# Optimization experiments

Hardware: AMD Instinct MI355X
Metric: run time of the kernel (lower is better)

## Reference

```python
import jax, jax.numpy as jnp
import numpy as np

NUM_NODES = 10000
NODE_DIM = 128
EDGE_DIM = 128
HIDDEN_DIM = 128
OUT_DIM = 128
N_EDGES = 640000


def setup_inputs() -> dict:
    key = jax.random.key(0)
    k = jax.random.split(key, 8)
    x = jax.random.normal(k[0], (NUM_NODES, NODE_DIM), dtype=jnp.float32)
    edge_index = jax.random.randint(k[1], (2, N_EDGES), 0, NUM_NODES, dtype=jnp.int64)
    edge_attr = jax.random.normal(k[2], (N_EDGES, EDGE_DIM), dtype=jnp.float32)
    # node2edge linear: in = 2*node_dim + edge_dim
    s1 = 1.0 / np.sqrt(2 * NODE_DIM + EDGE_DIM)
    W1 = jax.random.uniform(k[3], (2 * NODE_DIM + EDGE_DIM, HIDDEN_DIM), jnp.float32, -s1, s1)
    b1 = jax.random.uniform(k[4], (HIDDEN_DIM,), jnp.float32, -s1, s1)
    # edge2node linear: in = hidden_dim + node_dim
    s2 = 1.0 / np.sqrt(HIDDEN_DIM + NODE_DIM)
    W2 = jax.random.uniform(k[5], (HIDDEN_DIM + NODE_DIM, OUT_DIM), jnp.float32, -s2, s2)
    b2 = jax.random.uniform(k[6], (OUT_DIM,), jnp.float32, -s2, s2)
    return {"x": x, "edge_index": edge_index, "edge_attr": edge_attr,
            "W1": W1, "b1": b1, "W2": W2, "b2": b2}


def reference(x, edge_index, edge_attr, W1, b1, W2, b2):
    src, dst = edge_index[0], edge_index[1]
    # Node2Edge: gather endpoints, concat with edge features, linear
    h_i = x[src]                                   # [E, node_dim]
    h_j = x[dst]                                   # [E, node_dim]
    inp_e = jnp.concatenate([h_i, h_j, edge_attr], axis=-1)  # [E, 2*nd+ed]
    h_edge = inp_e @ W1 + b1                       # [E, hidden]
    # Edge2Node: scatter-sum edge embeddings to target nodes (edge_index[1])
    agg = jax.ops.segment_sum(h_edge, dst, num_segments=NUM_NODES)  # [N, hidden]
    inp_n = jnp.concatenate([agg, x], axis=-1)     # [N, hidden+nd]
    h_node = inp_n @ W2 + b2                       # [N, out]
    return h_node
```

## Files before the change

kernel.cpp:

```cpp
#include <hip/hip_runtime.h>


#define NN 10000
#define ED 640000
#define D  128
#define NB 64
#define EPB (ED / NB)

typedef __bf16 bf16;
typedef bf16  bf16x8 __attribute__((ext_vector_type(8)));
typedef float f32x4  __attribute__((ext_vector_type(4)));

__device__ __forceinline__ bf16 f2b(float f) {
  unsigned u = __builtin_bit_cast(unsigned, f);
  u += 0x7fffu + ((u >> 16) & 1u);
  unsigned short h = (unsigned short)(u >> 16);
  return __builtin_bit_cast(bf16, h);
}

__device__ __forceinline__ bf16x8 bzero8() {
  bf16 z = __builtin_bit_cast(bf16, (unsigned short)0);
  bf16x8 v = {z, z, z, z, z, z, z, z};
  return v;
}

__global__ __launch_bounds__(256) void k_prep(const float* __restrict__ x,
                                              const float* __restrict__ W1,
                                              const float* __restrict__ W2,
                                              bf16* __restrict__ xb,
                                              bf16* __restrict__ W1p,
                                              bf16* __restrict__ W2p) {
  int id = blockIdx.x * 256 + threadIdx.x;
  if (id < 160000) {
    int i = id * 8;
    f32x4 a = *(const f32x4*)(x + i);
    f32x4 b = *(const f32x4*)(x + i + 4);
    bf16x8 h;
    h[0]=f2b(a[0]); h[1]=f2b(a[1]); h[2]=f2b(a[2]); h[3]=f2b(a[3]);
    h[4]=f2b(b[0]); h[5]=f2b(b[1]); h[6]=f2b(b[2]); h[7]=f2b(b[3]);
    *(bf16x8*)(xb + i) = h;
  } else if (id < 166144) {
    int o8 = id - 160000;
    int kb = o8 >> 9, rem = o8 & 511, t = rem >> 6, L = rem & 63;
    int col  = t * 16 + (L & 15);
    int row0 = kb * 32 + (L >> 4) * 8;
    bf16x8 h;
    #pragma unroll
    for (int j = 0; j < 8; j++) h[j] = f2b(W1[(row0 + j) * D + col]);
    *(bf16x8*)(W1p + o8 * 8) = h;
  } else if (id < 170240) {
    int o8 = id - 166144;
    int kb = o8 >> 9, rem = o8 & 511, t = rem >> 6, L = rem & 63;
    int col  = t * 16 + (L & 15);
    int row0 = kb * 32 + (L >> 4) * 8;
    bf16x8 h;
    #pragma unroll
    for (int j = 0; j < 8; j++) h[j] = f2b(W2[(row0 + j) * D + col]);
    *(bf16x8*)(W2p + o8 * 8) = h;
  }
}

__global__ __launch_bounds__(256) void k_hist(const int* __restrict__ dst,
                                              int* __restrict__ hist) {
  __shared__ __align__(16) int h[NN];
  int b = blockIdx.x, tid = threadIdx.x;
  int4 z4 = make_int4(0, 0, 0, 0);
  for (int i = tid; i < NN / 4; i += 256) ((int4*)h)[i] = z4;
  __syncthreads();
  const int4* d4 = (const int4*)(dst + b * EPB);
  for (int i = tid; i < EPB / 4; i += 256) {
    int4 dd = d4[i];
    atomicAdd(&h[dd.x], 1);
    atomicAdd(&h[dd.y], 1);
    atomicAdd(&h[dd.z], 1);
    atomicAdd(&h[dd.w], 1);
  }
  __syncthreads();
  int4* outp = (int4*)(hist + (size_t)b * NN);
  for (int i = tid; i < NN / 4; i += 256) outp[i] = ((const int4*)h)[i];
}

__global__ __launch_bounds__(256) void k_colscan(int* __restrict__ hist,
                                                 int* __restrict__ counts) {
  int v = blockIdx.x * 256 + threadIdx.x;
  if (v >= NN) return;
  int run = 0;
  #pragma unroll
  for (int b = 0; b < NB; b++) {
    int t = hist[b * NN + v];
    hist[b * NN + v] = run;
    run += t;
  }
  counts[v] = run;
}

__global__ __launch_bounds__(256) void k_scan(const int* __restrict__ counts,
                                              int* __restrict__ row_ptr) {
  __shared__ int part[256];
  int tid = threadIdx.x;
  const int CH = 40;
  int base = tid * CH;
  int loc[CH];
  if (base + CH <= NN) {
    #pragma unroll
    for (int i = 0; i < CH / 4; i++) {
      int4 t = *(const int4*)(counts + base + i * 4);
      loc[i*4] = t.x; loc[i*4+1] = t.y; loc[i*4+2] = t.z; loc[i*4+3] = t.w;
    }
  } else {
    #pragma unroll
    for (int i = 0; i < CH; i++) loc[i] = (base + i < NN) ? counts[base + i] : 0;
  }
  int sum = 0;
  #pragma unroll
  for (int i = 0; i < CH; i++) sum += loc[i];
  part[tid] = sum;
  __syncthreads();
  for (int off = 1; off < 256; off <<= 1) {
    int v = (tid >= off) ? part[tid - off] : 0;
    __syncthreads();
    part[tid] += v;
    __syncthreads();
  }
  int run = part[tid] - sum;
  if (base + CH <= NN) {
    #pragma unroll
    for (int i = 0; i < CH / 4; i++) {
      int4 t;
      t.x = run; run += loc[i*4];
      t.y = run; run += loc[i*4+1];
      t.z = run; run += loc[i*4+2];
      t.w = run; run += loc[i*4+3];
      *(int4*)(row_ptr + base + i * 4) = t;
    }
  } else {
    #pragma unroll
    for (int i = 0; i < CH; i++) {
      int idx = base + i;
      if (idx < NN) { row_ptr[idx] = run; run += loc[i]; }
    }
  }
  if (tid == 255) row_ptr[NN] = part[255];
}

__global__ __launch_bounds__(256) void k_fill(const int* __restrict__ src,
                                              const int* __restrict__ dst,
                                              const int* __restrict__ row_ptr,
                                              const int* __restrict__ hist,
                                              int2* __restrict__ csr) {
  __shared__ __align__(16) int rk[NN];
  int b = blockIdx.x, tid = threadIdx.x;
  int4 z4 = make_int4(0, 0, 0, 0);
  for (int i = tid; i < NN / 4; i += 256) ((int4*)rk)[i] = z4;
  __syncthreads();
  int base = b * EPB;
  const int* __restrict__ hb = hist + (size_t)b * NN;
  const int4* d4 = (const int4*)(dst + base);
  const int4* s4 = (const int4*)(src + base);
  for (int i = tid; i < EPB / 4; i += 256) {
    int4 dd = d4[i];
    int4 ss = s4[i];
    int e = base + i * 4;
    {
      int r = atomicAdd(&rk[dd.x], 1);
      csr[row_ptr[dd.x] + hb[dd.x] + r] = make_int2(e + 0, ss.x);
    }
    {
      int r = atomicAdd(&rk[dd.y], 1);
      csr[row_ptr[dd.y] + hb[dd.y] + r] = make_int2(e + 1, ss.y);
    }
    {
      int r = atomicAdd(&rk[dd.z], 1);
      csr[row_ptr[dd.z] + hb[dd.z] + r] = make_int2(e + 2, ss.z);
    }
    {
      int r = atomicAdd(&rk[dd.w], 1);
      csr[row_ptr[dd.w] + hb[dd.w] + r] = make_int2(e + 3, ss.w);
    }
  }
}

__global__ __launch_bounds__(256) void k_sum(const bf16*  __restrict__ xb,
                                             const float* __restrict__ ea,
                                             const int*   __restrict__ row_ptr,
                                             const int2*  __restrict__ csr,
                                             float* __restrict__ sx,
                                             float* __restrict__ sea) {
  int gwave = (blockIdx.x * 256 + threadIdx.x) >> 6;
  if (gwave >= NN) return;
  int lane = threadIdx.x & 63;
  int g = lane >> 4, l = lane & 15;
  int e0 = row_ptr[gwave], e1 = row_ptr[gwave + 1];

  f32x4 ax0 = {0.f,0.f,0.f,0.f}, ax1 = {0.f,0.f,0.f,0.f};
  f32x4 ae0 = {0.f,0.f,0.f,0.f}, ae1 = {0.f,0.f,0.f,0.f};

  #pragma unroll 2
  for (int e = e0 + g; e < e1; e += 4) {
    long long cp = __builtin_nontemporal_load((const long long*)(csr + e));
    int2 es = __builtin_bit_cast(int2, cp);
    const f32x4* ep = (const f32x4*)(ea + (size_t)es.x * D + l * 8);
    f32x4 f0 = __builtin_nontemporal_load(ep);
    f32x4 f1 = __builtin_nontemporal_load(ep + 1);
    bf16x8 hx = *(const bf16x8*)(xb + (size_t)es.y * D + l * 8);
    ax0[0] += (float)hx[0]; ax0[1] += (float)hx[1];
    ax0[2] += (float)hx[2]; ax0[3] += (float)hx[3];
    ax1[0] += (float)hx[4]; ax1[1] += (float)hx[5];
    ax1[2] += (float)hx[6]; ax1[3] += (float)hx[7];
    ae0 += f0;
    ae1 += f1;
  }
  #pragma unroll
  for (int i = 0; i < 4; i++) {
    ax0[i] += __shfl_xor(ax0[i], 16, 64); ax0[i] += __shfl_xor(ax0[i], 32, 64);
    ax1[i] += __shfl_xor(ax1[i], 16, 64); ax1[i] += __shfl_xor(ax1[i], 32, 64);
    ae0[i] += __shfl_xor(ae0[i], 16, 64); ae0[i] += __shfl_xor(ae0[i], 32, 64);
    ae1[i] += __shfl_xor(ae1[i], 16, 64); ae1[i] += __shfl_xor(ae1[i], 32, 64);
  }
  if (lane < 16) {
    float* px = sx  + (size_t)gwave * D + l * 8;
    float* pe = sea + (size_t)gwave * D + l * 8;
    *(f32x4*)px       = ax0;
    *(f32x4*)(px + 4) = ax1;
    *(f32x4*)pe       = ae0;
    *(f32x4*)(pe + 4) = ae1;
  }
}

__global__ __launch_bounds__(256) void k_out(const float* __restrict__ sx,
                                             const float* __restrict__ sea,
                                             const bf16*  __restrict__ xb,
                                             const bf16*  __restrict__ W1p,
                                             const bf16*  __restrict__ W2p,
                                             const float* __restrict__ b1,
                                             const float* __restrict__ b2,
                                             const int*   __restrict__ row_ptr,
                                             float* __restrict__ out) {
  __shared__ __align__(16) bf16 lds[64 * 392];
  int tid  = threadIdx.x;
  int wave = tid >> 6, lane = tid & 63, quad = lane >> 4, l16 = lane & 15;
  int n0 = blockIdx.x * 64;

  #pragma unroll
  for (int i = 0; i < 4; i++) {
    int m = (tid >> 4) + 16 * i;
    int v = n0 + m;
    int cl = tid & 15;
    float cntf = (v < NN) ? (float)(row_ptr[v + 1] - row_ptr[v]) : 0.f;
    #pragma unroll
    for (int j = 0; j < 3; j++) {
      int c = cl + 16 * j;
      bf16x8 h;
      if (v < NN) {
        if (j == 0) {
          const float* p = sx + (size_t)v * D + cl * 8;
          f32x4 f0 = *(const f32x4*)p, f1 = *(const f32x4*)(p + 4);
          h[0]=f2b(f0[0]); h[1]=f2b(f0[1]); h[2]=f2b(f0[2]); h[3]=f2b(f0[3]);
          h[4]=f2b(f1[0]); h[5]=f2b(f1[1]); h[6]=f2b(f1[2]); h[7]=f2b(f1[3]);
        } else if (j == 1) {
          bf16x8 hx = *(const bf16x8*)(xb + (size_t)v * D + cl * 8);
          #pragma unroll
          for (int k = 0; k < 8; k++) h[k] = f2b((float)hx[k] * cntf);
        } else {
          const float* p = sea + (size_t)v * D + cl * 8;
          f32x4 f0 = *(const f32x4*)p, f1 = *(const f32x4*)(p + 4);
          h[0]=f2b(f0[0]); h[1]=f2b(f0[1]); h[2]=f2b(f0[2]); h[3]=f2b(f0[3]);
          h[4]=f2b(f1[0]); h[5]=f2b(f1[1]); h[6]=f2b(f1[2]); h[7]=f2b(f1[3]);
        }
      } else h = bzero8();
      *(bf16x8*)&lds[m * 392 + c * 8] = h;
    }
  }
  __syncthreads();

  f32x4 acc[4][2];
  #pragma unroll
  for (int mt = 0; mt < 4; mt++)
    #pragma unroll
    for (int tt = 0; tt < 2; tt++) acc[mt][tt] = (f32x4){0.f, 0.f, 0.f, 0.f};

  #pragma unroll
  for (int kb = 0; kb < 12; kb++) {
    bf16x8 B0 = *(const bf16x8*)(W1p + ((kb * 8 + wave * 2 + 0) * 64 + lane) * 8);
    bf16x8 B1 = *(const bf16x8*)(W1p + ((kb * 8 + wave * 2 + 1) * 64 + lane) * 8);
    #pragma unroll
    for (int mt = 0; mt < 4; mt++) {
      bf16x8 a = *(const bf16x8*)&lds[(mt * 16 + l16) * 392 + kb * 32 + quad * 8];
      acc[mt][0] = __builtin_amdgcn_mfma_f32_16x16x32_bf16(a, B0, acc[mt][0], 0, 0, 0);
      acc[mt][1] = __builtin_amdgcn_mfma_f32_16x16x32_bf16(a, B1, acc[mt][1], 0, 0, 0);
    }
  }
  __syncthreads();

  #pragma unroll
  for (int tt = 0; tt < 2; tt++) {
    int col = wave * 32 + tt * 16 + l16;
    float bb = b1[col];
    #pragma unroll
    for (int mt = 0; mt < 4; mt++)
      #pragma unroll
      for (int r = 0; r < 4; r++) {
        int m = mt * 16 + quad * 4 + r;
        int v = n0 + m;
        float cntf = (v < NN) ? (float)(row_ptr[v + 1] - row_ptr[v]) : 0.f;
        lds[m * 264 + col] = f2b(acc[mt][tt][r] + cntf * bb);
      }
  }
  #pragma unroll
  for (int i = 0; i < 4; i++) {
    int m = (tid >> 4) + 16 * i;
    int c = tid & 15;
    int v = n0 + m;
    bf16x8 h = (v < NN) ? *(const bf16x8*)(xb + (size_t)v * D + c * 8) : bzero8();
    *(bf16x8*)&lds[m * 264 + 128 + c * 8] = h;
  }
  __syncthreads();

  f32x4 acc2[4][2];
  #pragma unroll
  for (int mt = 0; mt < 4; mt++)
    #pragma unroll
    for (int tt = 0; tt < 2; tt++) acc2[mt][tt] = (f32x4){0.f, 0.f, 0.f, 0.f};

  #pragma unroll
  for (int kb = 0; kb < 8; kb++) {
    bf16x8 B0 = *(const bf16x8*)(W2p + ((kb * 8 + wave * 2 + 0) * 64 + lane) * 8);
    bf16x8 B1 = *(const bf16x8*)(W2p + ((kb * 8 + wave * 2 + 1) * 64 + lane) * 8);
    #pragma unroll
    for (int mt = 0; mt < 4; mt++) {
      bf16x8 a = *(const bf16x8*)&lds[(mt * 16 + l16) * 264 + kb * 32 + quad * 8];
      acc2[mt][0] = __builtin_amdgcn_mfma_f32_16x16x32_bf16(a, B0, acc2[mt][0], 0, 0, 0);
      acc2[mt][1] = __builtin_amdgcn_mfma_f32_16x16x32_bf16(a, B1, acc2[mt][1], 0, 0, 0);
    }
  }

  #pragma unroll
  for (int tt = 0; tt < 2; tt++) {
    int col = wave * 32 + tt * 16 + l16;
    float bb = b2[col];
    #pragma unroll
    for (int mt = 0; mt < 4; mt++)
      #pragma unroll
      for (int r = 0; r < 4; r++) {
        int v = n0 + mt * 16 + quad * 4 + r;
        if (v < NN) out[(size_t)v * D + col] = acc2[mt][tt][r] + bb;
      }
  }
}

extern "C" void kernel_launch(void* const* d_in, const int* in_sizes, int n_in,
                              void* d_out, int out_size, void* d_ws, size_t ws_size,
                              hipStream_t stream) {
  const float* x  = (const float*)d_in[0];
  const int*   ei = (const int*)  d_in[1];
  const float* ea = (const float*)d_in[2];
  const float* W1 = (const float*)d_in[3];
  const float* b1 = (const float*)d_in[4];
  const float* W2 = (const float*)d_in[5];
  const float* b2 = (const float*)d_in[6];
  float* out = (float*)d_out;

  char* ws = (char*)d_ws;
  size_t off = 0;
  auto alloc = [&](size_t bytes) -> void* {
    void* p = ws + off;
    off += (bytes + 255) & ~(size_t)255;
    return p;
  };
  bf16*  xb      = (bf16*)alloc((size_t)NN * D * 2);
  bf16*  W1p     = (bf16*)alloc(49152 * 2);
  bf16*  W2p     = (bf16*)alloc(32768 * 2);
  float* sx      = (float*)alloc((size_t)NN * D * 4);
  float* sea     = (float*)alloc((size_t)NN * D * 4);
  int*   counts  = (int*)alloc(NN * 4);
  int*   row_ptr = (int*)alloc((NN + 1) * 4);
  int*   hist    = (int*)alloc((size_t)NB * NN * 4);
  int2*  csr     = (int2*)alloc((size_t)ED * 8);
  (void)ws_size; (void)in_sizes; (void)n_in; (void)out_size;

  const int* src = ei;
  const int* dst = ei + ED;

  k_prep<<<665, 256, 0, stream>>>(x, W1, W2, xb, W1p, W2p);
  k_hist<<<NB, 256, 0, stream>>>(dst, hist);
  k_colscan<<<40, 256, 0, stream>>>(hist, counts);
  k_scan<<<1, 256, 0, stream>>>(counts, row_ptr);
  k_fill<<<NB, 256, 0, stream>>>(src, dst, row_ptr, hist, csr);
  k_sum<<<2500, 256, 0, stream>>>(xb, ea, row_ptr, csr, sx, sea);
  k_out<<<157, 256, 0, stream>>>(sx, sea, xb, W1p, W2p, b1, b2, row_ptr, out);
}
```

Baseline: 519.7 us.

## Fuse aggregation with output GEMMs and use fixed-stride padded CSR buckets

The neighbour-sum kernel and the output GEMM kernel are merged, so per-node sums go straight into LDS as bf16 instead of round-tripping through global fp32 sx/sea buffers. The global row_ptr scan kernel is removed by giving each node a fixed 192-slot CSR bucket, and the histogram pass is folded into the prep kernel to save launches. The padded layout assumes no node has more than 192 incoming edges; higher-degree inputs would corrupt memory. The fused kernel also runs far fewer waves on the latency-bound gather, which could hurt memory-level parallelism.

```diff
diff --git a/kernel.cpp b/kernel.cpp
--- a/kernel.cpp
+++ b/kernel.cpp
@@ -6,6 +6,7 @@
 #define D  128
 #define NB 64
 #define EPB (ED / NB)
+#define ST 192
 
 typedef __bf16 bf16;
 typedef bf16  bf16x8 __attribute__((ext_vector_type(8)));
@@ -24,60 +25,62 @@
   return v;
 }
 
-__global__ __launch_bounds__(256) void k_prep(const float* __restrict__ x,
-                                              const float* __restrict__ W1,
-                                              const float* __restrict__ W2,
-                                              bf16* __restrict__ xb,
-                                              bf16* __restrict__ W1p,
-                                              bf16* __restrict__ W2p) {
-  int id = blockIdx.x * 256 + threadIdx.x;
+__global__ __launch_bounds__(256) void k_prep_hist(const float* __restrict__ x,
+                                                   const float* __restrict__ W1,
+                                                   const float* __restrict__ W2,
+                                                   const int*   __restrict__ dst,
+                                                   bf16* __restrict__ xb,
+                                                   bf16* __restrict__ W1p,
+                                                   bf16* __restrict__ W2p,
+                                                   int*  __restrict__ hist) {
+  __shared__ __align__(16) int h[NN];
+  int tid = threadIdx.x;
+  if (blockIdx.x < NB) {
+    int b = blockIdx.x;
+    int4 z4 = make_int4(0, 0, 0, 0);
+    for (int i = tid; i < NN / 4; i += 256) ((int4*)h)[i] = z4;
+    __syncthreads();
+    const int4* d4 = (const int4*)(dst + b * EPB);
+    for (int i = tid; i < EPB / 4; i += 256) {
+      int4 dd = d4[i];
+      atomicAdd(&h[dd.x], 1);
+      atomicAdd(&h[dd.y], 1);
+      atomicAdd(&h[dd.z], 1);
+      atomicAdd(&h[dd.w], 1);
+    }
+    __syncthreads();
+    int4* outp = (int4*)(hist + (size_t)b * NN);
+    for (int i = tid; i < NN / 4; i += 256) outp[i] = ((const int4*)h)[i];
+    return;
+  }
+  int id = (blockIdx.x - NB) * 256 + tid;
   if (id < 160000) {
     int i = id * 8;
     f32x4 a = *(const f32x4*)(x + i);
     f32x4 b = *(const f32x4*)(x + i + 4);
-    bf16x8 h;
-    h[0]=f2b(a[0]); h[1]=f2b(a[1]); h[2]=f2b(a[2]); h[3]=f2b(a[3]);
-    h[4]=f2b(b[0]); h[5]=f2b(b[1]); h[6]=f2b(b[2]); h[7]=f2b(b[3]);
-    *(bf16x8*)(xb + i) = h;
+    bf16x8 hh;
+    hh[0]=f2b(a[0]); hh[1]=f2b(a[1]); hh[2]=f2b(a[2]); hh[3]=f2b(a[3]);
+    hh[4]=f2b(b[0]); hh[5]=f2b(b[1]); hh[6]=f2b(b[2]); hh[7]=f2b(b[3]);
+    *(bf16x8*)(xb + i) = hh;
   } else if (id < 166144) {
     int o8 = id - 160000;
     int kb = o8 >> 9, rem = o8 & 511, t = rem >> 6, L = rem & 63;
     int col  = t * 16 + (L & 15);
     int row0 = kb * 32 + (L >> 4) * 8;
-    bf16x8 h;
-    #pragma unroll
-    for (int j = 0; j < 8; j++) h[j] = f2b(W1[(row0 + j) * D + col]);
-    *(bf16x8*)(W1p + o8 * 8) = h;
+    bf16x8 hh;
+    #pragma unroll
+    for (int j = 0; j < 8; j++) hh[j] = f2b(W1[(row0 + j) * D + col]);
+    *(bf16x8*)(W1p + o8 * 8) = hh;
   } else if (id < 170240) {
     int o8 = id - 166144;
     int kb = o8 >> 9, rem = o8 & 511, t = rem >> 6, L = rem & 63;
     int col  = t * 16 + (L & 15);
     int row0 = kb * 32 + (L >> 4) * 8;
-    bf16x8 h;
-    #pragma unroll
-    for (int j = 0; j < 8; j++) h[j] = f2b(W2[(row0 + j) * D + col]);
-    *(bf16x8*)(W2p + o8 * 8) = h;
-  }
-}
-
-__global__ __launch_bounds__(256) void k_hist(const int* __restrict__ dst,
-                                              int* __restrict__ hist) {
-  __shared__ __align__(16) int h[NN];
-  int b = blockIdx.x, tid = threadIdx.x;
-  int4 z4 = make_int4(0, 0, 0, 0);
-  for (int i = tid; i < NN / 4; i += 256) ((int4*)h)[i] = z4;
-  __syncthreads();
-  const int4* d4 = (const int4*)(dst + b * EPB);
-  for (int i = tid; i < EPB / 4; i += 256) {
-    int4 dd = d4[i];
-    atomicAdd(&h[dd.x], 1);
-    atomicAdd(&h[dd.y], 1);
-    atomicAdd(&h[dd.z], 1);
-    atomicAdd(&h[dd.w], 1);
-  }
-  __syncthreads();
-  int4* outp = (int4*)(hist + (size_t)b * NN);
-  for (int i = tid; i < NN / 4; i += 256) outp[i] = ((const int4*)h)[i];
+    bf16x8 hh;
+    #pragma unroll
+    for (int j = 0; j < 8; j++) hh[j] = f2b(W2[(row0 + j) * D + col]);
+    *(bf16x8*)(W2p + o8 * 8) = hh;
+  }
 }
 
 __global__ __launch_bounds__(256) void k_colscan(int* __restrict__ hist,
@@ -94,58 +97,8 @@
   counts[v] = run;
 }
 
-__global__ __launch_bounds__(256) void k_scan(const int* __restrict__ counts,
-                                              int* __restrict__ row_ptr) {
-  __shared__ int part[256];
-  int tid = threadIdx.x;
-  const int CH = 40;
-  int base = tid * CH;
-  int loc[CH];
-  if (base + CH <= NN) {
-    #pragma unroll
-    for (int i = 0; i < CH / 4; i++) {
-      int4 t = *(const int4*)(counts + base + i * 4);
-      loc[i*4] = t.x; loc[i*4+1] = t.y; loc[i*4+2] = t.z; loc[i*4+3] = t.w;
-    }
-  } else {
-    #pragma unroll
-    for (int i = 0; i < CH; i++) loc[i] = (base + i < NN) ? counts[base + i] : 0;
-  }
-  int sum = 0;
-  #pragma unroll
-  for (int i = 0; i < CH; i++) sum += loc[i];
-  part[tid] = sum;
-  __syncthreads();
-  for (int off = 1; off < 256; off <<= 1) {
-    int v = (tid >= off) ? part[tid - off] : 0;
-    __syncthreads();
-    part[tid] += v;
-    __syncthreads();
-  }
-  int run = part[tid] - sum;
-  if (base + CH <= NN) {
-    #pragma unroll
-    for (int i = 0; i < CH / 4; i++) {
-      int4 t;
-      t.x = run; run += loc[i*4];
-      t.y = run; run += loc[i*4+1];
-      t.z = run; run += loc[i*4+2];
-      t.w = run; run += loc[i*4+3];
-      *(int4*)(row_ptr + base + i * 4) = t;
-    }
-  } else {
-    #pragma unroll
-    for (int i = 0; i < CH; i++) {
-      int idx = base + i;
-      if (idx < NN) { row_ptr[idx] = run; run += loc[i]; }
-    }
-  }
-  if (tid == 255) row_ptr[NN] = part[255];
-}
-
 __global__ __launch_bounds__(256) void k_fill(const int* __restrict__ src,
                                               const int* __restrict__ dst,
-                                              const int* __restrict__ row_ptr,
                                               const int* __restrict__ hist,
                                               int2* __restrict__ csr) {
   __shared__ __align__(16) int rk[NN];
@@ -163,188 +116,145 @@
     int e = base + i * 4;
     {
       int r = atomicAdd(&rk[dd.x], 1);
-      csr[row_ptr[dd.x] + hb[dd.x] + r] = make_int2(e + 0, ss.x);
+      csr[(size_t)dd.x * ST + hb[dd.x] + r] = make_int2(e + 0, ss.x);
     }
     {
       int r = atomicAdd(&rk[dd.y], 1);
-      csr[row_ptr[dd.y] + hb[dd.y] + r] = make_int2(e + 1, ss.y);
+      csr[(size_t)dd.y * ST + hb[dd.y] + r] = make_int2(e + 1, ss.y);
     }
     {
       int r = atomicAdd(&rk[dd.z], 1);
-      csr[row_ptr[dd.z] + hb[dd.z] + r] = make_int2(e + 2, ss.z);
+      csr[(size_t)dd.z * ST + hb[dd.z] + r] = make_int2(e + 2, ss.z);
     }
     {
       int r = atomicAdd(&rk[dd.w], 1);
-      csr[row_ptr[dd.w] + hb[dd.w] + r] = make_int2(e + 3, ss.w);
-    }
-  }
-}
-
-__global__ __launch_bounds__(256) void k_sum(const bf16*  __restrict__ xb,
-                                             const float* __restrict__ ea,
-                                             const int*   __restrict__ row_ptr,
-                                             const int2*  __restrict__ csr,
-                                             float* __restrict__ sx,
-                                             float* __restrict__ sea) {
-  int gwave = (blockIdx.x * 256 + threadIdx.x) >> 6;
-  if (gwave >= NN) return;
-  int lane = threadIdx.x & 63;
-  int g = lane >> 4, l = lane & 15;
-  int e0 = row_ptr[gwave], e1 = row_ptr[gwave + 1];
-
-  f32x4 ax0 = {0.f,0.f,0.f,0.f}, ax1 = {0.f,0.f,0.f,0.f};
-  f32x4 ae0 = {0.f,0.f,0.f,0.f}, ae1 = {0.f,0.f,0.f,0.f};
-
-  #pragma unroll 2
-  for (int e = e0 + g; e < e1; e += 4) {
-    long long cp = __builtin_nontemporal_load((const long long*)(csr + e));
-    int2 es = __builtin_bit_cast(int2, cp);
-    const f32x4* ep = (const f32x4*)(ea + (size_t)es.x * D + l * 8);
-    f32x4 f0 = __builtin_nontemporal_load(ep);
-    f32x4 f1 = __builtin_nontemporal_load(ep + 1);
-    bf16x8 hx = *(const bf16x8*)(xb + (size_t)es.y * D + l * 8);
-    ax0[0] += (float)hx[0]; ax0[1] += (float)hx[1];
-    ax0[2] += (float)hx[2]; ax0[3] += (float)hx[3];
-    ax1[0] += (float)hx[4]; ax1[1] += (float)hx[5];
-    ax1[2] += (float)hx[6]; ax1[3] += (float)hx[7];
-    ae0 += f0;
-    ae1 += f1;
-  }
-  #pragma unroll
-  for (int i = 0; i < 4; i++) {
-    ax0[i] += __shfl_xor(ax0[i], 16, 64); ax0[i] += __shfl_xor(ax0[i], 32, 64);
-    ax1[i] += __shfl_xor(ax1[i], 16, 64); ax1[i] += __shfl_xor(ax1[i], 32, 64);
-    ae0[i] += __shfl_xor(ae0[i], 16, 64); ae0[i] += __shfl_xor(ae0[i], 32, 64);
-    ae1[i] += __shfl_xor(ae1[i], 16, 64); ae1[i] += __shfl_xor(ae1[i], 32, 64);
-  }
-  if (lane < 16) {
-    float* px = sx  + (size_t)gwave * D + l * 8;
-    float* pe = sea + (size_t)gwave * D + l * 8;
-    *(f32x4*)px       = ax0;
-    *(f32x4*)(px + 4) = ax1;
-    *(f32x4*)pe       = ae0;
-    *(f32x4*)(pe + 4) = ae1;
-  }
-}
-
-__global__ __launch_bounds__(256) void k_out(const float* __restrict__ sx,
-                                             const float* __restrict__ sea,
-                                             const bf16*  __restrict__ xb,
-                                             const bf16*  __restrict__ W1p,
-                                             const bf16*  __restrict__ W2p,
-                                             const float* __restrict__ b1,
-                                             const float* __restrict__ b2,
-                                             const int*   __restrict__ row_ptr,
-                                             float* __restrict__ out) {
-  __shared__ __align__(16) bf16 lds[64 * 392];
+      csr[(size_t)dd.w * ST + hb[dd.w] + r] = make_int2(e + 3, ss.w);
+    }
+  }
+}
+
+__global__ __launch_bounds__(512, 6) void k_sumout(const bf16*  __restrict__ xb,
+                                                   const float* __restrict__ ea,
+                                                   const int*   __restrict__ counts,
+                                                   const int2*  __restrict__ csr,
+                                                   const bf16*  __restrict__ W1p,
+                                                   const bf16*  __restrict__ W2p,
+                                                   const float* __restrict__ b1,
+                                                   const float* __restrict__ b2,
+                                                   float* __restrict__ out) {
+  __shared__ __align__(16) bf16 lds[32 * 392];
   int tid  = threadIdx.x;
-  int wave = tid >> 6, lane = tid & 63, quad = lane >> 4, l16 = lane & 15;
-  int n0 = blockIdx.x * 64;
-
-  #pragma unroll
-  for (int i = 0; i < 4; i++) {
-    int m = (tid >> 4) + 16 * i;
+  int w = tid >> 6, lane = tid & 63, quad = lane >> 4, l16 = lane & 15;
+  int g = quad, l = l16;
+  int n0 = blockIdx.x * 32;
+
+  for (int q = 0; q < 4; q++) {
+    int m = w * 4 + q;
     int v = n0 + m;
-    int cl = tid & 15;
-    float cntf = (v < NN) ? (float)(row_ptr[v + 1] - row_ptr[v]) : 0.f;
-    #pragma unroll
-    for (int j = 0; j < 3; j++) {
-      int c = cl + 16 * j;
+    int cnt = (v < NN) ? counts[v] : 0;
+    f32x4 ax0 = {0.f,0.f,0.f,0.f}, ax1 = {0.f,0.f,0.f,0.f};
+    f32x4 ae0 = {0.f,0.f,0.f,0.f}, ae1 = {0.f,0.f,0.f,0.f};
+    const int2* cbase = csr + (size_t)v * ST;
+    #pragma unroll 2
+    for (int e = g; e < cnt; e += 4) {
+      long long cp = __builtin_nontemporal_load((const long long*)(cbase + e));
+      int2 es = __builtin_bit_cast(int2, cp);
+      const f32x4* ep = (const f32x4*)(ea + (size_t)es.x * D + l * 8);
+      f32x4 f0 = __builtin_nontemporal_load(ep);
+      f32x4 f1 = __builtin_nontemporal_load(ep + 1);
+      bf16x8 hx = *(const bf16x8*)(xb + (size_t)es.y * D + l * 8);
+      ax0[0] += (float)hx[0]; ax0[1] += (float)hx[1];
+      ax0[2] += (float)hx[2]; ax0[3] += (float)hx[3];
+      ax1[0] += (float)hx[4]; ax1[1] += (float)hx[5];
+      ax1[2] += (float)hx[6]; ax1[3] += (float)hx[7];
+      ae0 += f0;
+      ae1 += f1;
+    }
+    #pragma unroll
+    for (int i = 0; i < 4; i++) {
+      ax0[i] += __shfl_xor(ax0[i], 16, 64); ax0[i] += __shfl_xor(ax0[i], 32, 64);
+      ax1[i] += __shfl_xor(ax1[i], 16, 64); ax1[i] += __shfl_xor(ax1[i], 32, 64);
+      ae0[i] += __shfl_xor(ae0[i], 16, 64); ae0[i] += __shfl_xor(ae0[i], 32, 64);
+      ae1[i] += __shfl_xor(ae1[i], 16, 64); ae1[i] += __shfl_xor(ae1[i], 32, 64);
+    }
+    if (g == 0) {
       bf16x8 h;
-      if (v < NN) {
-        if (j == 0) {
-          const float* p = sx + (size_t)v * D + cl * 8;
-          f32x4 f0 = *(const f32x4*)p, f1 = *(const f32x4*)(p + 4);
-          h[0]=f2b(f0[0]); h[1]=f2b(f0[1]); h[2]=f2b(f0[2]); h[3]=f2b(f0[3]);
-          h[4]=f2b(f1[0]); h[5]=f2b(f1[1]); h[6]=f2b(f1[2]); h[7]=f2b(f1[3]);
-        } else if (j == 1) {
-          bf16x8 hx = *(const bf16x8*)(xb + (size_t)v * D + cl * 8);
-          #pragma unroll
-          for (int k = 0; k < 8; k++) h[k] = f2b((float)hx[k] * cntf);
-        } else {
-          const float* p = sea + (size_t)v * D + cl * 8;
-          f32x4 f0 = *(const f32x4*)p, f1 = *(const f32x4*)(p + 4);
-          h[0]=f2b(f0[0]); h[1]=f2b(f0[1]); h[2]=f2b(f0[2]); h[3]=f2b(f0[3]);
-          h[4]=f2b(f1[0]); h[5]=f2b(f1[1]); h[6]=f2b(f1[2]); h[7]=f2b(f1[3]);
-        }
-      } else h = bzero8();
-      *(bf16x8*)&lds[m * 392 + c * 8] = h;
-    }
-  }
-  __syncthreads();
-
-  f32x4 acc[4][2];
-  #pragma unroll
-  for (int mt = 0; mt < 4; mt++)
-    #pragma unroll
-    for (int tt = 0; tt < 2; tt++) acc[mt][tt] = (f32x4){0.f, 0.f, 0.f, 0.f};
-
+      h[0]=f2b(ax0[0]); h[1]=f2b(ax0[1]); h[2]=f2b(ax0[2]); h[3]=f2b(ax0[3]);
+      h[4]=f2b(ax1[0]); h[5]=f2b(ax1[1]); h[6]=f2b(ax1[2]); h[7]=f2b(ax1[3]);
+      *(bf16x8*)&lds[m * 392 + l * 8] = h;
+    } else if (g == 1) {
+      bf16x8 h;
+      h[0]=f2b(ae0[0]); h[1]=f2b(ae0[1]); h[2]=f2b(ae0[2]); h[3]=f2b(ae0[3]);
+      h[4]=f2b(ae1[0]); h[5]=f2b(ae1[1]); h[6]=f2b(ae1[2]); h[7]=f2b(ae1[3]);
+      *(bf16x8*)&lds[m * 392 + 256 + l * 8] = h;
+    } else if (g == 2) {
+      float cntf = (float)cnt;
+      bf16x8 hx = (v < NN) ? *(const bf16x8*)(xb + (size_t)v * D + l * 8) : bzero8();
+      bf16x8 h;
+      #pragma unroll
+      for (int k = 0; k < 8; k++) h[k] = f2b((float)hx[k] * cntf);
+      *(bf16x8*)&lds[m * 392 + 128 + l * 8] = h;
+    }
+  }
+  __syncthreads();
+
+  int mh = w >> 2, nc = w & 3;
+  f32x4 acc0 = {0.f,0.f,0.f,0.f}, acc1 = {0.f,0.f,0.f,0.f};
   #pragma unroll
   for (int kb = 0; kb < 12; kb++) {
-    bf16x8 B0 = *(const bf16x8*)(W1p + ((kb * 8 + wave * 2 + 0) * 64 + lane) * 8);
-    bf16x8 B1 = *(const bf16x8*)(W1p + ((kb * 8 + wave * 2 + 1) * 64 + lane) * 8);
-    #pragma unroll
-    for (int mt = 0; mt < 4; mt++) {
-      bf16x8 a = *(const bf16x8*)&lds[(mt * 16 + l16) * 392 + kb * 32 + quad * 8];
-      acc[mt][0] = __builtin_amdgcn_mfma_f32_16x16x32_bf16(a, B0, acc[mt][0], 0, 0, 0);
-      acc[mt][1] = __builtin_amdgcn_mfma_f32_16x16x32_bf16(a, B1, acc[mt][1], 0, 0, 0);
-    }
-  }
-  __syncthreads();
-
+    bf16x8 B0 = *(const bf16x8*)(W1p + ((kb * 8 + nc * 2 + 0) * 64 + lane) * 8);
+    bf16x8 B1 = *(const bf16x8*)(W1p + ((kb * 8 + nc * 2 + 1) * 64 + lane) * 8);
+    bf16x8 a = *(const bf16x8*)&lds[(mh * 16 + l16) * 392 + kb * 32 + quad * 8];
+    acc0 = __builtin_amdgcn_mfma_f32_16x16x32_bf16(a, B0, acc0, 0, 0, 0);
+    acc1 = __builtin_amdgcn_mfma_f32_16x16x32_bf16(a, B1, acc1, 0, 0, 0);
+  }
+  __syncthreads();
+
+  float cr[4];
+  #pragma unroll
+  for (int r = 0; r < 4; r++) {
+    int v = n0 + mh * 16 + quad * 4 + r;
+    cr[r] = (v < NN) ? (float)counts[v] : 0.f;
+  }
   #pragma unroll
   for (int tt = 0; tt < 2; tt++) {
-    int col = wave * 32 + tt * 16 + l16;
+    int col = nc * 32 + tt * 16 + l16;
     float bb = b1[col];
-    #pragma unroll
-    for (int mt = 0; mt < 4; mt++)
-      #pragma unroll
-      for (int r = 0; r < 4; r++) {
-        int m = mt * 16 + quad * 4 + r;
-        int v = n0 + m;
-        float cntf = (v < NN) ? (float)(row_ptr[v + 1] - row_ptr[v]) : 0.f;
-        lds[m * 264 + col] = f2b(acc[mt][tt][r] + cntf * bb);
-      }
-  }
-  #pragma unroll
-  for (int i = 0; i < 4; i++) {
-    int m = (tid >> 4) + 16 * i;
-    int c = tid & 15;
-    int v = n0 + m;
-    bf16x8 h = (v < NN) ? *(const bf16x8*)(xb + (size_t)v * D + c * 8) : bzero8();
-    *(bf16x8*)&lds[m * 264 + 128 + c * 8] = h;
-  }
-  __syncthreads();
-
-  f32x4 acc2[4][2];
-  #pragma unroll
-  for (int mt = 0; mt < 4; mt++)
-    #pragma unroll
-    for (int tt = 0; tt < 2; tt++) acc2[mt][tt] = (f32x4){0.f, 0.f, 0.f, 0.f};
-
+    f32x4 av = tt ? acc1 : acc0;
+    #pragma unroll
+    for (int r = 0; r < 4; r++) {
+      int m = mh * 16 + quad * 4 + r;
+      lds[m * 264 + col] = f2b(av[r] + cr[r] * bb);
+    }
+  }
+  {
+    int m2 = tid >> 4, c = tid & 15;
+    int v2 = n0 + m2;
+    bf16x8 h = (v2 < NN) ? *(const bf16x8*)(xb + (size_t)v2 * D + c * 8) : bzero8();
+    *(bf16x8*)&lds[m2 * 264 + 128 + c * 8] = h;
+  }
+  __syncthreads();
+
+  f32x4 acc2a = {0.f,0.f,0.f,0.f}, acc2b = {0.f,0.f,0.f,0.f};
   #pragma unroll
   for (int kb = 0; kb < 8; kb++) {
-    bf16x8 B0 = *(const bf16x8*)(W2p + ((kb * 8 + wave * 2 + 0) * 64 + lane) * 8);
-    bf16x8 B1 = *(const bf16x8*)(W2p + ((kb * 8 + wave * 2 + 1) * 64 + lane) * 8);
-    #pragma unroll
-    for (int mt = 0; mt < 4; mt++) {
-      bf16x8 a = *(const bf16x8*)&lds[(mt * 16 + l16) * 264 + kb * 32 + quad * 8];
-      acc2[mt][0] = __builtin_amdgcn_mfma_f32_16x16x32_bf16(a, B0, acc2[mt][0], 0, 0, 0);
-      acc2[mt][1] = __builtin_amdgcn_mfma_f32_16x16x32_bf16(a, B1, acc2[mt][1], 0, 0, 0);
-    }
+    bf16x8 B0 = *(const bf16x8*)(W2p + ((kb * 8 + nc * 2 + 0) * 64 + lane) * 8);
+    bf16x8 B1 = *(const bf16x8*)(W2p + ((kb * 8 + nc * 2 + 1) * 64 + lane) * 8);
+    bf16x8 a = *(const bf16x8*)&lds[(mh * 16 + l16) * 264 + kb * 32 + quad * 8];
+    acc2a = __builtin_amdgcn_mfma_f32_16x16x32_bf16(a, B0, acc2a, 0, 0, 0);
+    acc2b = __builtin_amdgcn_mfma_f32_16x16x32_bf16(a, B1, acc2b, 0, 0, 0);
   }
 
   #pragma unroll
   for (int tt = 0; tt < 2; tt++) {
-    int col = wave * 32 + tt * 16 + l16;
+    int col = nc * 32 + tt * 16 + l16;
     float bb = b2[col];
-    #pragma unroll
-    for (int mt = 0; mt < 4; mt++)
-      #pragma unroll
-      for (int r = 0; r < 4; r++) {
-        int v = n0 + mt * 16 + quad * 4 + r;
-        if (v < NN) out[(size_t)v * D + col] = acc2[mt][tt][r] + bb;
-      }
+    f32x4 av = tt ? acc2b : acc2a;
+    #pragma unroll
+    for (int r = 0; r < 4; r++) {
+      int v = n0 + mh * 16 + quad * 4 + r;
+      if (v < NN) out[(size_t)v * D + col] = av[r] + bb;
+    }
   }
 }
 
@@ -370,22 +280,16 @@
   bf16*  xb      = (bf16*)alloc((size_t)NN * D * 2);
   bf16*  W1p     = (bf16*)alloc(49152 * 2);
   bf16*  W2p     = (bf16*)alloc(32768 * 2);
-  float* sx      = (float*)alloc((size_t)NN * D * 4);
-  float* sea     = (float*)alloc((size_t)NN * D * 4);
   int*   counts  = (int*)alloc(NN * 4);
-  int*   row_ptr = (int*)alloc((NN + 1) * 4);
   int*   hist    = (int*)alloc((size_t)NB * NN * 4);
-  int2*  csr     = (int2*)alloc((size_t)ED * 8);
+  int2*  csr     = (int2*)alloc((size_t)NN * ST * 8);
   (void)ws_size; (void)in_sizes; (void)n_in; (void)out_size;
 
   const int* src = ei;
   const int* dst = ei + ED;
 
-  k_prep<<<665, 256, 0, stream>>>(x, W1, W2, xb, W1p, W2p);
-  k_hist<<<NB, 256, 0, stream>>>(dst, hist);
+  k_prep_hist<<<NB + 665, 256, 0, stream>>>(x, W1, W2, dst, xb, W1p, W2p, hist);
   k_colscan<<<40, 256, 0, stream>>>(hist, counts);
-  k_scan<<<1, 256, 0, stream>>>(counts, row_ptr);
-  k_fill<<<NB, 256, 0, stream>>>(src, dst, row_ptr, hist, csr);
-  k_sum<<<2500, 256, 0, stream>>>(xb, ea, row_ptr, csr, sx, sea);
-  k_out<<<157, 256, 0, stream>>>(sx, sea, xb, W1p, W2p, b1, b2, row_ptr, out);
-}
+  k_fill<<<NB, 256, 0, stream>>>(src, dst, hist, csr);
+  k_sumout<<<313, 512, 0, stream>>>(xb, ea, counts, csr, W1p, W2p, b1, b2, out);
+}
```

Result: slower. 550.1 us (+5.9%).
